# Kernel tuning notes

Measured on AMD Instinct MI355X. Metric: run time of the kernel, lower is better.

The kernel has to match this reference:

```python
import jax, jax.numpy as jnp
import numpy as np

N = 50000
E_RAND = 800000
IN_CH = 128
HID = 64
HEADS = 4
OUT_CH = 3
NEG_SLOPE = 0.2
BN_EPS = 1e-5


def setup_inputs() -> dict:
    key = jax.random.key(0)
    ks = jax.random.split(key, 24)
    x = jax.random.normal(ks[0], (N, IN_CH), dtype=jnp.float32)
    er = jax.random.randint(ks[1], (2, E_RAND), 0, N)
    sl = jnp.tile(jnp.arange(N, dtype=er.dtype)[None, :], (2, 1))
    edge_index = jnp.concatenate([er, sl], axis=1)  # [2, 850000]
    s = 0.1
    d1 = HID * HEADS            # 256
    d2 = (HID // 2) * HEADS     # 128
    inp = dict(x=x, edge_index=edge_index)
    # layer 1: in 128 -> heads*64
    inp["W1"] = s * jax.random.normal(ks[2], (IN_CH, HEADS * HID), dtype=jnp.float32)
    inp["a1s"] = s * jax.random.normal(ks[3], (HEADS, HID), dtype=jnp.float32)
    inp["a1d"] = s * jax.random.normal(ks[4], (HEADS, HID), dtype=jnp.float32)
    inp["b1"] = jnp.zeros((d1,), jnp.float32)
    inp["g1"] = jnp.ones((d1,), jnp.float32)
    inp["be1"] = jnp.zeros((d1,), jnp.float32)
    inp["m1"] = 0.01 * jax.random.normal(ks[5], (d1,), dtype=jnp.float32)
    inp["v1"] = jnp.ones((d1,), jnp.float32) + 0.01 * jax.random.uniform(ks[6], (d1,))
    # layer 2: in 256 -> heads*32
    inp["W2"] = s * jax.random.normal(ks[7], (d1, HEADS * (HID // 2)), dtype=jnp.float32)
    inp["a2s"] = s * jax.random.normal(ks[8], (HEADS, HID // 2), dtype=jnp.float32)
    inp["a2d"] = s * jax.random.normal(ks[9], (HEADS, HID // 2), dtype=jnp.float32)
    inp["b2"] = jnp.zeros((d2,), jnp.float32)
    inp["g2"] = jnp.ones((d2,), jnp.float32)
    inp["be2"] = jnp.zeros((d2,), jnp.float32)
    inp["m2"] = 0.01 * jax.random.normal(ks[10], (d2,), dtype=jnp.float32)
    inp["v2"] = jnp.ones((d2,), jnp.float32) + 0.01 * jax.random.uniform(ks[11], (d2,))
    # layer 3: in 128 -> 1 head, out_ch, concat=False
    inp["W3"] = s * jax.random.normal(ks[12], (d2, OUT_CH), dtype=jnp.float32)
    inp["a3s"] = s * jax.random.normal(ks[13], (1, OUT_CH), dtype=jnp.float32)
    inp["a3d"] = s * jax.random.normal(ks[14], (1, OUT_CH), dtype=jnp.float32)
    inp["b3"] = jnp.zeros((OUT_CH,), jnp.float32)
    return inp


def gat_conv(x, src, dst, W, a_src, a_dst, b, heads, fdim, concat):
    n = x.shape[0]
    h = (x @ W).reshape(n, heads, fdim)           # [N,H,F]
    als = jnp.einsum('nhf,hf->nh', h, a_src)      # [N,H]
    ald = jnp.einsum('nhf,hf->nh', h, a_dst)
    e = jax.nn.leaky_relu(als[src] + ald[dst], NEG_SLOPE)  # [E,H]
    m = jax.lax.stop_gradient(jax.ops.segment_max(e, dst, num_segments=n))
    ex = jnp.exp(e - m[dst])
    ssum = jax.ops.segment_sum(ex, dst, num_segments=n)
    alpha = ex / (ssum[dst] + 1e-16)              # segment softmax over in-edges
    msg = h[src] * alpha[:, :, None]              # [E,H,F]
    out = jax.ops.segment_sum(msg, dst, num_segments=n)  # [N,H,F]
    out = out.reshape(n, heads * fdim) if concat else out.mean(axis=1)
    return out + b


def batch_norm(x, gamma, beta, mean, var):
    return (x - mean) * jax.lax.rsqrt(var + BN_EPS) * gamma + beta


def reference(x, edge_index, W1, a1s, a1d, b1, g1, be1, m1, v1,
              W2, a2s, a2d, b2, g2, be2, m2, v2,
              W3, a3s, a3d, b3):
    src, dst = edge_index[0], edge_index[1]
    h = gat_conv(x, src, dst, W1, a1s, a1d, b1, HEADS, HID, True)
    h = jax.nn.elu(batch_norm(h, g1, be1, m1, v1))
    h = gat_conv(h, src, dst, W2, a2s, a2d, b2, HEADS, HID // 2, True)
    h = jax.nn.elu(batch_norm(h, g2, be2, m2, v2))
    h = gat_conv(h, src, dst, W3, a3s, a3d, b3, 1, OUT_CH, False)
    return jax.nn.log_softmax(h, axis=1)
```

## Files before the change

kernel.cpp:

```cpp
#include <hip/hip_runtime.h>


#define WSZ 64

typedef short short8 __attribute__((ext_vector_type(8)));
typedef short short4v __attribute__((ext_vector_type(4)));
typedef float float4v __attribute__((ext_vector_type(4)));

__device__ inline unsigned short f2bf(float f) {
  unsigned u = __float_as_uint(f);
  u += 0x7FFFu + ((u >> 16) & 1u);
  return (unsigned short)(u >> 16);
}
__device__ inline float bf2f(unsigned short u) {
  return __uint_as_float(((unsigned)u) << 16);
}


__global__ __launch_bounds__(256) void hist_kernel(const int* __restrict__ dst, int E,
                                                   int* __restrict__ deg) {
  int e = blockIdx.x * 256 + threadIdx.x;
  if (e < E) atomicAdd(&deg[dst[e]], 1);
}

__global__ __launch_bounds__(256) void block_sums_kernel(const int* __restrict__ deg, int n,
                                                         int* __restrict__ bsum) {
  __shared__ int sh[256];
  int t = threadIdx.x;
  int base = blockIdx.x * 1024 + t * 4;
  int v = 0;
#pragma unroll
  for (int j = 0; j < 4; ++j) {
    int idx = base + j;
    if (idx < n) v += deg[idx];
  }
  sh[t] = v;
  __syncthreads();
  for (int off = 128; off >= 1; off >>= 1) {
    if (t < off) sh[t] += sh[t + off];
    __syncthreads();
  }
  if (t == 0) bsum[blockIdx.x] = sh[0];
}

__global__ void tiny_scan_kernel(int* bsum, int nb) {
  if (threadIdx.x == 0 && blockIdx.x == 0) {
    int run = 0;
    for (int i = 0; i < nb; ++i) {
      int v = bsum[i];
      bsum[i] = run;
      run += v;
    }
  }
}

__global__ __launch_bounds__(256) void scan_write_kernel(const int* __restrict__ deg, int n,
                                                         const int* __restrict__ bbase,
                                                         int* __restrict__ row_start,
                                                         int* __restrict__ cursor) {
  __shared__ int sh[256];
  int t = threadIdx.x;
  int base = blockIdx.x * 1024 + t * 4;
  int v[4];
  int s = 0;
#pragma unroll
  for (int j = 0; j < 4; ++j) {
    int idx = base + j;
    v[j] = (idx < n) ? deg[idx] : 0;
    s += v[j];
  }
  sh[t] = s;
  __syncthreads();
  for (int off = 1; off < 256; off <<= 1) {
    int x = (t >= off) ? sh[t - off] : 0;
    __syncthreads();
    sh[t] += x;
    __syncthreads();
  }
  int excl = sh[t] - s + bbase[blockIdx.x];
#pragma unroll
  for (int j = 0; j < 4; ++j) {
    int idx = base + j;
    if (idx < n) {
      row_start[idx] = excl;
      cursor[idx] = excl;
    }
    excl += v[j];
  }
  if (blockIdx.x == gridDim.x - 1 && t == 255) row_start[n] = excl;
}

__global__ __launch_bounds__(256) void scatter_kernel(const int* __restrict__ src,
                                                      const int* __restrict__ dst, int E,
                                                      int* __restrict__ cursor,
                                                      int* __restrict__ csr_src) {
  int e = blockIdx.x * 256 + threadIdx.x;
  if (e < E) {
    int d = dst[e];
    int p = atomicAdd(&cursor[d], 1);
    csr_src[p] = src[e];
  }
}


__global__ __launch_bounds__(256) void conv_w1t_kernel(const float* __restrict__ W1,
                                                       unsigned short* __restrict__ W1t) {
  int idx = blockIdx.x * 256 + threadIdx.x;
  int n = idx >> 7, k = idx & 127;
  W1t[idx] = f2bf(W1[k * 256 + n]);
}

__global__ __launch_bounds__(256) void conv_w2t_kernel(const float* __restrict__ W2,
                                                       unsigned short* __restrict__ W2t) {
  int idx = blockIdx.x * 256 + threadIdx.x;
  int n = idx >> 8, p = idx & 255;
  int kl = (p & ~63) | ((p & 3) << 4) | ((p >> 2) & 15);
  W2t[idx] = f2bf(W2[kl * 128 + n]);
}


template <int K, int BN, bool AF32>
__global__ __launch_bounds__(256) void gemm_mfma(
    const void* __restrict__ Ap,
    const unsigned short* __restrict__ Bt,
    const float* __restrict__ a_s, const float* __restrict__ a_d,
    unsigned short* __restrict__ hout,
    float* __restrict__ als, float* __restrict__ ald,
    int M) {
  constexpr int CF = BN / 64;
  constexpr int PAD = 36;
  __shared__ unsigned short As[64][PAD];
  __shared__ unsigned short Bs[BN][PAD];
  const int t = threadIdx.x;
  const int w = t >> 6;
  const int lane = t & 63;
  const int c16 = lane & 15;
  const int q = lane >> 4;
  const int bm = blockIdx.x * 64;
  const int arow = t >> 2;
  const int akc = (t & 3) * 8;

  float4v acc[4][CF];
#pragma unroll
  for (int rf = 0; rf < 4; ++rf)
#pragma unroll
    for (int cf = 0; cf < CF; ++cf) acc[rf][cf] = float4v{0.f, 0.f, 0.f, 0.f};

  for (int k0 = 0; k0 < K; k0 += 32) {
    {
      int gr = bm + arow;
      if constexpr (AF32) {
        const float* Af = (const float*)Ap + (size_t)gr * K + k0 + akc;
        float4 v0 = make_float4(0.f, 0.f, 0.f, 0.f), v1 = v0;
        if (gr < M) {
          v0 = *(const float4*)Af;
          v1 = *(const float4*)(Af + 4);
        }
        ushort4 u0, u1;
        u0.x = f2bf(v0.x); u0.y = f2bf(v0.y); u0.z = f2bf(v0.z); u0.w = f2bf(v0.w);
        u1.x = f2bf(v1.x); u1.y = f2bf(v1.y); u1.z = f2bf(v1.z); u1.w = f2bf(v1.w);
        *(ushort4*)&As[arow][akc] = u0;
        *(ushort4*)&As[arow][akc + 4] = u1;
      } else {
        uint4 v = make_uint4(0u, 0u, 0u, 0u);
        if (gr < M) v = *(const uint4*)((const unsigned short*)Ap + (size_t)gr * K + k0 + akc);
        *(uint2*)&As[arow][akc] = make_uint2(v.x, v.y);
        *(uint2*)&As[arow][akc + 4] = make_uint2(v.z, v.w);
      }
    }
#pragma unroll
    for (int h = 0; h < BN / 64; ++h) {
      int n = (t >> 2) + h * 64;
      uint4 v = *(const uint4*)(Bt + (size_t)n * K + k0 + akc);
      *(uint2*)&Bs[n][akc] = make_uint2(v.x, v.y);
      *(uint2*)&Bs[n][akc + 4] = make_uint2(v.z, v.w);
    }
    __syncthreads();
    short8 af[4], bfr[CF];
#pragma unroll
    for (int rf = 0; rf < 4; ++rf) {
      short4v lo = *(short4v*)&As[rf * 16 + c16][q * 8];
      short4v hi = *(short4v*)&As[rf * 16 + c16][q * 8 + 4];
      af[rf] = __builtin_shufflevector(lo, hi, 0, 1, 2, 3, 4, 5, 6, 7);
    }
#pragma unroll
    for (int cf = 0; cf < CF; ++cf) {
      int n = w * (CF * 16) + cf * 16 + c16;
      short4v lo = *(short4v*)&Bs[n][q * 8];
      short4v hi = *(short4v*)&Bs[n][q * 8 + 4];
      bfr[cf] = __builtin_shufflevector(lo, hi, 0, 1, 2, 3, 4, 5, 6, 7);
    }
#pragma unroll
    for (int rf = 0; rf < 4; ++rf)
#pragma unroll
      for (int cf = 0; cf < CF; ++cf)
        acc[rf][cf] =
            __builtin_amdgcn_mfma_f32_16x16x32_bf16(af[rf], bfr[cf], acc[rf][cf], 0, 0, 0);
    __syncthreads();
  }

  float sasv[CF], sadv[CF];
#pragma unroll
  for (int cf = 0; cf < CF; ++cf) {
    int L = w * (CF * 16) + cf * 16 + c16;
    sasv[cf] = a_s[L];
    sadv[cf] = a_d[L];
  }
#pragma unroll
  for (int rf = 0; rf < 4; ++rf) {
#pragma unroll
    for (int r = 0; r < 4; ++r) {
      int n = bm + rf * 16 + q * 4 + r;
      float ps = 0.f, pd = 0.f;
      unsigned short us[CF];
#pragma unroll
      for (int cf = 0; cf < CF; ++cf) {
        float v = acc[rf][cf][r];
        us[cf] = f2bf(v);
        ps += v * sasv[cf];
        pd += v * sadv[cf];
      }
#pragma unroll
      for (int off = 1; off <= 8; off <<= 1) {
        ps += __shfl_xor(ps, off, 16);
        pd += __shfl_xor(pd, off, 16);
      }
      if (n < M) {
        if constexpr (CF == 4) {
          ushort4 u;
          u.x = us[0]; u.y = us[1]; u.z = us[2]; u.w = us[3];
          *(ushort4*)(hout + (size_t)n * BN + w * 64 + c16 * 4) = u;
        } else {
          ushort2 u;
          u.x = us[0]; u.y = us[1];
          *(ushort2*)(hout + (size_t)n * BN + w * 32 + c16 * 2) = u;
        }
        if (c16 == 0) {
          als[(size_t)n * 4 + w] = ps;
          ald[(size_t)n * 4 + w] = pd;
        }
      }
    }
  }
}


template <int D, bool FUSEL3>
__global__ __launch_bounds__(256) void gat_aggregate(
    const unsigned short* __restrict__ h_bf, const float* __restrict__ als,
    const float* __restrict__ ald, const int* __restrict__ row_start,
    const int* __restrict__ csr_src, const float* __restrict__ bias,
    const float* __restrict__ gamma, const float* __restrict__ beta,
    const float* __restrict__ bmean, const float* __restrict__ bvar,
    unsigned short* __restrict__ obf,
    const float* __restrict__ W3, const float* __restrict__ a3s,
    const float* __restrict__ a3d, float4* __restrict__ h3p,
    float* __restrict__ ald3,
    int n_nodes) {
  constexpr int VPT = D / WSZ;
  constexpr int H = 4;
  __shared__ float w3s[384];
  __shared__ float sa3[6];
  if constexpr (FUSEL3) {
    for (int i = threadIdx.x; i < 384; i += 256) w3s[i] = W3[i];
    if (threadIdx.x < 3) {
      sa3[threadIdx.x] = a3s[threadIdx.x];
      sa3[3 + threadIdx.x] = a3d[threadIdx.x];
    }
    __syncthreads();
  }
  int wid = threadIdx.x >> 6, lane = threadIdx.x & 63;
  int n = __builtin_amdgcn_readfirstlane(blockIdx.x * 4 + wid);
  if (n >= n_nodes) return;
  int hd = lane >> 4;
  const unsigned coff = (unsigned)(lane * VPT * 2);
  const unsigned aoff = (unsigned)(hd * 4);
  const char* hb = (const char*)h_bf;
  const char* ab = (const char*)als;
  float aldv = ald[(size_t)n * H + hd];
  int row = __builtin_amdgcn_readfirstlane(row_start[n]);
  int end = __builtin_amdgcn_readfirstlane(row_start[n + 1]);
  float acc[VPT] = {};
  float ssum = 0.f;
  int i = row;

#define EDGE_BLOCK(B)                                                          \
  for (; i + (B) <= end; i += (B)) {                                           \
    int s[B];                                                                  \
    _Pragma("unroll") for (int j = 0; j < (B); ++j) s[j] =                     \
        __builtin_amdgcn_readfirstlane(csr_src[i + j]);                        \
    float e[B];                                                                \
    _Pragma("unroll") for (int j = 0; j < (B); ++j) e[j] =                     \
        *(const float*)(ab + ((unsigned)s[j] * 16u + aoff)) + aldv;            \
    if constexpr (VPT == 4) {                                                  \
      ushort4 u[B];                                                            \
      _Pragma("unroll") for (int j = 0; j < (B); ++j) u[j] =                   \
          *(const ushort4*)(hb + ((unsigned)s[j] * (unsigned)(D * 2) + coff)); \
      _Pragma("unroll") for (int j = 0; j < (B); ++j) {                        \
        float ee = fmaxf(e[j], 0.2f * e[j]);                                   \
        float ex = __expf(ee);                                                 \
        ssum += ex;                                                            \
        acc[0] += ex * bf2f(u[j].x);                                           \
        acc[1] += ex * bf2f(u[j].y);                                           \
        acc[2] += ex * bf2f(u[j].z);                                           \
        acc[3] += ex * bf2f(u[j].w);                                           \
      }                                                                        \
    } else {                                                                   \
      ushort2 u[B];                                                            \
      _Pragma("unroll") for (int j = 0; j < (B); ++j) u[j] =                   \
          *(const ushort2*)(hb + ((unsigned)s[j] * (unsigned)(D * 2) + coff)); \
      _Pragma("unroll") for (int j = 0; j < (B); ++j) {                        \
        float ee = fmaxf(e[j], 0.2f * e[j]);                                   \
        float ex = __expf(ee);                                                 \
        ssum += ex;                                                            \
        acc[0] += ex * bf2f(u[j].x);                                           \
        acc[1] += ex * bf2f(u[j].y);                                           \
      }                                                                        \
    }                                                                          \
  }

  EDGE_BLOCK(8)
  EDGE_BLOCK(4)
  EDGE_BLOCK(1)
#undef EDGE_BLOCK

  float inv = 1.f / (ssum + 1e-16f);
#pragma unroll
  for (int j = 0; j < VPT; ++j) {
    int cl = hd * (VPT * 16) + j * 16 + (lane & 15);
    float o = acc[j] * inv + bias[cl];
    o = (o - bmean[cl]) * rsqrtf(bvar[cl] + 1e-5f) * gamma[cl] + beta[cl];
    o = (o > 0.f) ? o : (__expf(o) - 1.f);
    acc[j] = o;
  }
  if constexpr (!FUSEL3) {
    ushort4 u;
    u.x = f2bf(acc[0]); u.y = f2bf(acc[1]); u.z = f2bf(acc[2]); u.w = f2bf(acc[3]);
    *(ushort4*)(obf + (size_t)n * D + (lane * VPT)) = u;
  } else {
    int k0l = hd * 32 + (lane & 15);
    int k1l = k0l + 16;
    float p0 = acc[0] * w3s[k0l * 3 + 0] + acc[1] * w3s[k1l * 3 + 0];
    float p1 = acc[0] * w3s[k0l * 3 + 1] + acc[1] * w3s[k1l * 3 + 1];
    float p2 = acc[0] * w3s[k0l * 3 + 2] + acc[1] * w3s[k1l * 3 + 2];
#pragma unroll
    for (int off = 32; off >= 1; off >>= 1) {
      p0 += __shfl_xor(p0, off, 64);
      p1 += __shfl_xor(p1, off, 64);
      p2 += __shfl_xor(p2, off, 64);
    }
    if (lane == 0) {
      float als3 = p0 * sa3[0] + p1 * sa3[1] + p2 * sa3[2];
      float ad3 = p0 * sa3[3] + p1 * sa3[4] + p2 * sa3[5];
      h3p[n] = make_float4(p0, p1, p2, als3);
      ald3[n] = ad3;
    }
  }
}


__global__ __launch_bounds__(256) void l3_agg_kernel(const float4* __restrict__ h3p,
                                                     const float* __restrict__ ald3,
                                                     const int* __restrict__ row_start,
                                                     const int* __restrict__ csr_src,
                                                     const float* __restrict__ b3,
                                                     float* __restrict__ out, int n_nodes) {
  int wid = threadIdx.x >> 6, lane = threadIdx.x & 63;
  int n = __builtin_amdgcn_readfirstlane(blockIdx.x * 4 + wid);
  if (n >= n_nodes) return;
  float aldv = ald3[n];
  int row = __builtin_amdgcn_readfirstlane(row_start[n]);
  int end = __builtin_amdgcn_readfirstlane(row_start[n + 1]);
  const char* hp = (const char*)h3p;
  float a0 = 0.f, a1 = 0.f, a2 = 0.f, ss = 0.f;
  for (int i = row + lane; i < end; i += 64) {
    int s = csr_src[i];
    float4 hv = *(const float4*)(hp + ((unsigned)s * 16u));
    float e = hv.w + aldv;
    e = fmaxf(e, 0.2f * e);
    float ex = __expf(e);
    ss += ex;
    a0 += ex * hv.x;
    a1 += ex * hv.y;
    a2 += ex * hv.z;
  }
#pragma unroll
  for (int off = 32; off >= 1; off >>= 1) {
    a0 += __shfl_xor(a0, off, 64);
    a1 += __shfl_xor(a1, off, 64);
    a2 += __shfl_xor(a2, off, 64);
    ss += __shfl_xor(ss, off, 64);
  }
  if (lane == 0) {
    float inv = 1.f / (ss + 1e-16f);
    float o0 = a0 * inv + b3[0];
    float o1 = a1 * inv + b3[1];
    float o2 = a2 * inv + b3[2];
    float m = fmaxf(o0, fmaxf(o1, o2));
    float lse = m + logf(expf(o0 - m) + expf(o1 - m) + expf(o2 - m));
    out[n * 3 + 0] = o0 - lse;
    out[n * 3 + 1] = o1 - lse;
    out[n * 3 + 2] = o2 - lse;
  }
}


extern "C" void kernel_launch(void* const* d_in, const int* in_sizes, int n_in,
                              void* d_out, int out_size, void* d_ws, size_t ws_size,
                              hipStream_t stream) {
  const float* x   = (const float*)d_in[0];
  const int*   ei  = (const int*)d_in[1];
  const float* W1  = (const float*)d_in[2];
  const float* a1s = (const float*)d_in[3];
  const float* a1d = (const float*)d_in[4];
  const float* b1  = (const float*)d_in[5];
  const float* g1v = (const float*)d_in[6];
  const float* be1 = (const float*)d_in[7];
  const float* m1  = (const float*)d_in[8];
  const float* v1  = (const float*)d_in[9];
  const float* W2  = (const float*)d_in[10];
  const float* a2s = (const float*)d_in[11];
  const float* a2d = (const float*)d_in[12];
  const float* b2  = (const float*)d_in[13];
  const float* g2v = (const float*)d_in[14];
  const float* be2 = (const float*)d_in[15];
  const float* m2  = (const float*)d_in[16];
  const float* v2  = (const float*)d_in[17];
  const float* W3  = (const float*)d_in[18];
  const float* a3s = (const float*)d_in[19];
  const float* a3d = (const float*)d_in[20];
  const float* b3  = (const float*)d_in[21];
  float* out = (float*)d_out;

  const int N = in_sizes[0] / 128;
  const int E = in_sizes[1] / 2;
  const int* srcv = ei;
  const int* dstv = ei + E;

  float* wsf  = (float*)d_ws;
  float* als1 = wsf;
  float* ald1 = als1 + (size_t)N * 4;
  float* als2 = ald1 + (size_t)N * 4;
  float* ald2 = als2 + (size_t)N * 4;
  float* h3p  = ald2 + (size_t)N * 4;
  float* ald3 = h3p + (size_t)N * 4;
  unsigned short* h_bf1 = (unsigned short*)(ald3 + N);
  unsigned short* o1_bf = h_bf1 + (size_t)N * 256;
  unsigned short* h_bf2 = o1_bf + (size_t)N * 256;
  unsigned short* W1t   = h_bf2 + (size_t)N * 128;
  unsigned short* W2t   = W1t + 256 * 128;
  int* deg       = (int*)(W2t + 128 * 256);
  int* row_start = deg + N;
  int* cursor    = row_start + (N + 1);
  int* csr_src   = cursor + (N + 1);
  int* bsum      = csr_src + E;

  const int eb = (E + 255) / 256;
  const int nb = (N + 1023) / 1024;
  const int nodes4 = (N + 3) / 4;
  const int mblocks = (N + 63) / 64;

  conv_w1t_kernel<<<128, 256, 0, stream>>>(W1, W1t);
  conv_w2t_kernel<<<128, 256, 0, stream>>>(W2, W2t);

  hipMemsetAsync(deg, 0, (size_t)N * sizeof(int), stream);
  hist_kernel<<<eb, 256, 0, stream>>>(dstv, E, deg);
  block_sums_kernel<<<nb, 256, 0, stream>>>(deg, N, bsum);
  tiny_scan_kernel<<<1, 64, 0, stream>>>(bsum, nb);
  scan_write_kernel<<<nb, 256, 0, stream>>>(deg, N, bsum, row_start, cursor);
  scatter_kernel<<<eb, 256, 0, stream>>>(srcv, dstv, E, cursor, csr_src);

  gemm_mfma<128, 256, true><<<mblocks, 256, 0, stream>>>(x, W1t, a1s, a1d, h_bf1, als1,
                                                         ald1, N);
  gat_aggregate<256, false><<<nodes4, 256, 0, stream>>>(
      h_bf1, als1, ald1, row_start, csr_src, b1, g1v, be1, m1, v1, o1_bf, nullptr, nullptr,
      nullptr, nullptr, nullptr, N);
  gemm_mfma<256, 128, false><<<mblocks, 256, 0, stream>>>(o1_bf, W2t, a2s, a2d, h_bf2, als2,
                                                          ald2, N);
  gat_aggregate<128, true><<<nodes4, 256, 0, stream>>>(
      h_bf2, als2, ald2, row_start, csr_src, b2, g2v, be2, m2, v2, nullptr, W3, a3s, a3d,
      (float4*)h3p, ald3, N);
  l3_agg_kernel<<<nodes4, 256, 0, stream>>>((const float4*)h3p, ald3, row_start, csr_src,
                                            b3, out, N);
}
```

Measured before the change: 385.9 us.

## Store GAT features as feature slices and aggregate per slice block

The GEMM epilogue now writes hidden features into 8 feature-slice planes, each contiguous per node. The aggregation kernels assign each block one slice and a group of 8 nodes, processing several edges in parallel per wave with lane groups, so gathers touch a smaller working set that may fit in cache. Layer-3 prep is split into a separate kernel that reads an fp32 intermediate. The cost is redundant reads of CSR and attention logits across 8 slices, plus an extra kernel and an fp32 round trip.

```diff
diff --git a/kernel.cpp b/kernel.cpp
--- a/kernel.cpp
+++ b/kernel.cpp
@@ -6,6 +6,7 @@
 typedef short short8 __attribute__((ext_vector_type(8)));
 typedef short short4v __attribute__((ext_vector_type(4)));
 typedef float float4v __attribute__((ext_vector_type(4)));
+typedef float f2v __attribute__((ext_vector_type(2)));
 
 __device__ inline unsigned short f2bf(float f) {
   unsigned u = __float_as_uint(f);
@@ -128,6 +129,7 @@
     float* __restrict__ als, float* __restrict__ ald,
     int M) {
   constexpr int CF = BN / 64;
+  constexpr int SF = BN / 8;
   constexpr int PAD = 36;
   __shared__ unsigned short As[64][PAD];
   __shared__ unsigned short Bs[BN][PAD];
@@ -206,6 +208,7 @@
     sasv[cf] = a_s[L];
     sadv[cf] = a_d[L];
   }
+  const size_t sub = (size_t)(w * 2 + (c16 >> 3)) * (size_t)M * SF;
 #pragma unroll
   for (int rf = 0; rf < 4; ++rf) {
 #pragma unroll
@@ -229,11 +232,11 @@
         if constexpr (CF == 4) {
           ushort4 u;
           u.x = us[0]; u.y = us[1]; u.z = us[2]; u.w = us[3];
-          *(ushort4*)(hout + (size_t)n * BN + w * 64 + c16 * 4) = u;
+          *(ushort4*)(hout + sub + (size_t)n * 32 + (c16 & 7) * 4) = u;
         } else {
           ushort2 u;
           u.x = us[0]; u.y = us[1];
-          *(ushort2*)(hout + (size_t)n * BN + w * 32 + c16 * 2) = u;
+          *(ushort2*)(hout + sub + (size_t)n * 16 + (c16 & 7) * 2) = u;
         }
         if (c16 == 0) {
           als[(size_t)n * 4 + w] = ps;
@@ -245,116 +248,128 @@
 }
 
 
-template <int D, bool FUSEL3>
-__global__ __launch_bounds__(256) void gat_aggregate(
-    const unsigned short* __restrict__ h_bf, const float* __restrict__ als,
-    const float* __restrict__ ald, const int* __restrict__ row_start,
-    const int* __restrict__ csr_src, const float* __restrict__ bias,
-    const float* __restrict__ gamma, const float* __restrict__ beta,
-    const float* __restrict__ bmean, const float* __restrict__ bvar,
+template <int D>
+__global__ __launch_bounds__(256) void gat_agg_slice(
+    const unsigned short* __restrict__ h_sl,
+    const float* __restrict__ als, const float* __restrict__ ald,
+    const int* __restrict__ row_start, const int* __restrict__ csr_src,
+    const float* __restrict__ bias, const float* __restrict__ gamma,
+    const float* __restrict__ beta, const float* __restrict__ bmean,
+    const float* __restrict__ bvar,
     unsigned short* __restrict__ obf,
-    const float* __restrict__ W3, const float* __restrict__ a3s,
-    const float* __restrict__ a3d, float4* __restrict__ h3p,
-    float* __restrict__ ald3,
+    float* __restrict__ of32,
     int n_nodes) {
-  constexpr int VPT = D / WSZ;
-  constexpr int H = 4;
+  constexpr int SFEAT = (D == 256) ? 32 : 16;
+  constexpr int FP = SFEAT / 2;
+  constexpr int EPG = 64 / FP;
+  const int b = blockIdx.x;
+  const int sl = b & 7;
+  const int g = b >> 3;
+  const int wid = threadIdx.x >> 6;
+  const int lane = threadIdx.x & 63;
+  const int f = lane & (FP - 1);
+  const int eg = lane >> ((D == 256) ? 4 : 3);
+  const int head = sl >> 1;
+  const char* hsb = (const char*)(h_sl + (size_t)sl * (size_t)n_nodes * SFEAT);
+  const char* ab = (const char*)als;
+
+  for (int rep = 0; rep < 2; ++rep) {
+    int n = __builtin_amdgcn_readfirstlane(g * 8 + wid + rep * 4);
+    if (n >= n_nodes) continue;
+    float aldv = ald[(size_t)n * 4 + head];
+    int row = __builtin_amdgcn_readfirstlane(row_start[n]);
+    int end = __builtin_amdgcn_readfirstlane(row_start[n + 1]);
+    float acc0 = 0.f, acc1 = 0.f, ssum = 0.f;
+    for (int i = row; i < end; i += EPG) {
+      int idx = i + eg;
+      idx = (idx < end) ? idx : (end - 1);
+      int s = __builtin_nontemporal_load(&csr_src[idx]);
+      float al = *(const float*)(ab + ((unsigned)s * 16u + (unsigned)(head * 4)));
+      unsigned u = *(const unsigned*)(hsb + ((unsigned)s * (unsigned)(SFEAT * 2) +
+                                             (unsigned)(f * 4)));
+      float e = al + aldv;
+      e = fmaxf(e, 0.2f * e);
+      float ex = __expf(e);
+      ex = (i + eg < end) ? ex : 0.f;
+      ssum += ex;
+      acc0 += ex * __uint_as_float(u << 16);
+      acc1 += ex * __uint_as_float(u & 0xffff0000u);
+    }
+    if constexpr (EPG == 8) {
+      ssum += __shfl_xor(ssum, 8, 64);
+      acc0 += __shfl_xor(acc0, 8, 64);
+      acc1 += __shfl_xor(acc1, 8, 64);
+    }
+    ssum += __shfl_xor(ssum, 16, 64);
+    acc0 += __shfl_xor(acc0, 16, 64);
+    acc1 += __shfl_xor(acc1, 16, 64);
+    ssum += __shfl_xor(ssum, 32, 64);
+    acc0 += __shfl_xor(acc0, 32, 64);
+    acc1 += __shfl_xor(acc1, 32, 64);
+    float inv = 1.f / (ssum + 1e-16f);
+    int l0, l1;
+    if constexpr (D == 256) {
+      l0 = head * 64 + ((f & 1) * 2 + 0) * 16 + (sl & 1) * 8 + (f >> 1);
+      l1 = head * 64 + ((f & 1) * 2 + 1) * 16 + (sl & 1) * 8 + (f >> 1);
+    } else {
+      l0 = head * 32 + (sl & 1) * 8 + f;
+      l1 = l0 + 16;
+    }
+    float o0 = acc0 * inv + bias[l0];
+    o0 = (o0 - bmean[l0]) * rsqrtf(bvar[l0] + 1e-5f) * gamma[l0] + beta[l0];
+    o0 = (o0 > 0.f) ? o0 : (__expf(o0) - 1.f);
+    float o1v = acc1 * inv + bias[l1];
+    o1v = (o1v - bmean[l1]) * rsqrtf(bvar[l1] + 1e-5f) * gamma[l1] + beta[l1];
+    o1v = (o1v > 0.f) ? o1v : (__expf(o1v) - 1.f);
+    if (eg == 0) {
+      if constexpr (D == 256) {
+        unsigned pk = (unsigned)f2bf(o0) | ((unsigned)f2bf(o1v) << 16);
+        __builtin_nontemporal_store(
+            pk, (unsigned*)(obf + (size_t)n * 256 + sl * 32 + f * 2));
+      } else {
+        f2v v2;
+        v2.x = o0; v2.y = o1v;
+        __builtin_nontemporal_store(
+            v2, (f2v*)(of32 + (size_t)n * 128 + sl * 16 + f * 2));
+      }
+    }
+  }
+}
+
+
+__global__ __launch_bounds__(256) void l3_prep_kernel(
+    const float* __restrict__ o2, const float* __restrict__ W3,
+    const float* __restrict__ a3s, const float* __restrict__ a3d,
+    float4* __restrict__ h3p, float* __restrict__ ald3, int n_nodes) {
   __shared__ float w3s[384];
   __shared__ float sa3[6];
-  if constexpr (FUSEL3) {
-    for (int i = threadIdx.x; i < 384; i += 256) w3s[i] = W3[i];
-    if (threadIdx.x < 3) {
-      sa3[threadIdx.x] = a3s[threadIdx.x];
-      sa3[3 + threadIdx.x] = a3d[threadIdx.x];
-    }
-    __syncthreads();
-  }
+  for (int i = threadIdx.x; i < 384; i += 256) w3s[i] = W3[i];
+  if (threadIdx.x < 3) {
+    sa3[threadIdx.x] = a3s[threadIdx.x];
+    sa3[3 + threadIdx.x] = a3d[threadIdx.x];
+  }
+  __syncthreads();
   int wid = threadIdx.x >> 6, lane = threadIdx.x & 63;
-  int n = __builtin_amdgcn_readfirstlane(blockIdx.x * 4 + wid);
+  int n = blockIdx.x * 4 + wid;
   if (n >= n_nodes) return;
+  f2v v = *(const f2v*)(o2 + (size_t)n * 128 + lane * 2);
   int hd = lane >> 4;
-  const unsigned coff = (unsigned)(lane * VPT * 2);
-  const unsigned aoff = (unsigned)(hd * 4);
-  const char* hb = (const char*)h_bf;
-  const char* ab = (const char*)als;
-  float aldv = ald[(size_t)n * H + hd];
-  int row = __builtin_amdgcn_readfirstlane(row_start[n]);
-  int end = __builtin_amdgcn_readfirstlane(row_start[n + 1]);
-  float acc[VPT] = {};
-  float ssum = 0.f;
-  int i = row;
-
-#define EDGE_BLOCK(B)                                                          \
-  for (; i + (B) <= end; i += (B)) {                                           \
-    int s[B];                                                                  \
-    _Pragma("unroll") for (int j = 0; j < (B); ++j) s[j] =                     \
-        __builtin_amdgcn_readfirstlane(csr_src[i + j]);                        \
-    float e[B];                                                                \
-    _Pragma("unroll") for (int j = 0; j < (B); ++j) e[j] =                     \
-        *(const float*)(ab + ((unsigned)s[j] * 16u + aoff)) + aldv;            \
-    if constexpr (VPT == 4) {                                                  \
-      ushort4 u[B];                                                            \
-      _Pragma("unroll") for (int j = 0; j < (B); ++j) u[j] =                   \
-          *(const ushort4*)(hb + ((unsigned)s[j] * (unsigned)(D * 2) + coff)); \
-      _Pragma("unroll") for (int j = 0; j < (B); ++j) {                        \
-        float ee = fmaxf(e[j], 0.2f * e[j]);                                   \
-        float ex = __expf(ee);                                                 \
-        ssum += ex;                                                            \
-        acc[0] += ex * bf2f(u[j].x);                                           \
-        acc[1] += ex * bf2f(u[j].y);                                           \
-        acc[2] += ex * bf2f(u[j].z);                                           \
-        acc[3] += ex * bf2f(u[j].w);                                           \
-      }                                                                        \
-    } else {                                                                   \
-      ushort2 u[B];                                                            \
-      _Pragma("unroll") for (int j = 0; j < (B); ++j) u[j] =                   \
-          *(const ushort2*)(hb + ((unsigned)s[j] * (unsigned)(D * 2) + coff)); \
-      _Pragma("unroll") for (int j = 0; j < (B); ++j) {                        \
-        float ee = fmaxf(e[j], 0.2f * e[j]);                                   \
-        float ex = __expf(ee);                                                 \
-        ssum += ex;                                                            \
-        acc[0] += ex * bf2f(u[j].x);                                           \
-        acc[1] += ex * bf2f(u[j].y);                                           \
-      }                                                                        \
-    }                                                                          \
-  }
-
-  EDGE_BLOCK(8)
-  EDGE_BLOCK(4)
-  EDGE_BLOCK(1)
-#undef EDGE_BLOCK
-
-  float inv = 1.f / (ssum + 1e-16f);
-#pragma unroll
-  for (int j = 0; j < VPT; ++j) {
-    int cl = hd * (VPT * 16) + j * 16 + (lane & 15);
-    float o = acc[j] * inv + bias[cl];
-    o = (o - bmean[cl]) * rsqrtf(bvar[cl] + 1e-5f) * gamma[cl] + beta[cl];
-    o = (o > 0.f) ? o : (__expf(o) - 1.f);
-    acc[j] = o;
-  }
-  if constexpr (!FUSEL3) {
-    ushort4 u;
-    u.x = f2bf(acc[0]); u.y = f2bf(acc[1]); u.z = f2bf(acc[2]); u.w = f2bf(acc[3]);
-    *(ushort4*)(obf + (size_t)n * D + (lane * VPT)) = u;
-  } else {
-    int k0l = hd * 32 + (lane & 15);
-    int k1l = k0l + 16;
-    float p0 = acc[0] * w3s[k0l * 3 + 0] + acc[1] * w3s[k1l * 3 + 0];
-    float p1 = acc[0] * w3s[k0l * 3 + 1] + acc[1] * w3s[k1l * 3 + 1];
-    float p2 = acc[0] * w3s[k0l * 3 + 2] + acc[1] * w3s[k1l * 3 + 2];
-#pragma unroll
-    for (int off = 32; off >= 1; off >>= 1) {
-      p0 += __shfl_xor(p0, off, 64);
-      p1 += __shfl_xor(p1, off, 64);
-      p2 += __shfl_xor(p2, off, 64);
-    }
-    if (lane == 0) {
-      float als3 = p0 * sa3[0] + p1 * sa3[1] + p2 * sa3[2];
-      float ad3 = p0 * sa3[3] + p1 * sa3[4] + p2 * sa3[5];
-      h3p[n] = make_float4(p0, p1, p2, als3);
-      ald3[n] = ad3;
-    }
+  int k0l = hd * 32 + (lane & 15);
+  int k1l = k0l + 16;
+  float p0 = v.x * w3s[k0l * 3 + 0] + v.y * w3s[k1l * 3 + 0];
+  float p1 = v.x * w3s[k0l * 3 + 1] + v.y * w3s[k1l * 3 + 1];
+  float p2 = v.x * w3s[k0l * 3 + 2] + v.y * w3s[k1l * 3 + 2];
+#pragma unroll
+  for (int off = 32; off >= 1; off >>= 1) {
+    p0 += __shfl_xor(p0, off, 64);
+    p1 += __shfl_xor(p1, off, 64);
+    p2 += __shfl_xor(p2, off, 64);
+  }
+  if (lane == 0) {
+    float als3 = p0 * sa3[0] + p1 * sa3[1] + p2 * sa3[2];
+    float ad3 = p0 * sa3[3] + p1 * sa3[4] + p2 * sa3[5];
+    h3p[n] = make_float4(p0, p1, p2, als3);
+    ald3[n] = ad3;
   }
 }
 
@@ -444,21 +459,23 @@
   float* ald2 = als2 + (size_t)N * 4;
   float* h3p  = ald2 + (size_t)N * 4;
   float* ald3 = h3p + (size_t)N * 4;
-  unsigned short* h_bf1 = (unsigned short*)(ald3 + N);
-  unsigned short* o1_bf = h_bf1 + (size_t)N * 256;
-  unsigned short* h_bf2 = o1_bf + (size_t)N * 256;
-  unsigned short* W1t   = h_bf2 + (size_t)N * 128;
+  unsigned short* h1s   = (unsigned short*)(ald3 + N);
+  unsigned short* o1_bf = h1s + (size_t)N * 256;
+  unsigned short* h2s   = o1_bf + (size_t)N * 256;
+  unsigned short* W1t   = h2s + (size_t)N * 128;
   unsigned short* W2t   = W1t + 256 * 128;
   int* deg       = (int*)(W2t + 128 * 256);
   int* row_start = deg + N;
   int* cursor    = row_start + (N + 1);
   int* csr_src   = cursor + (N + 1);
   int* bsum      = csr_src + E;
+  float* o2f = (float*)h1s;
 
   const int eb = (E + 255) / 256;
   const int nb = (N + 1023) / 1024;
   const int nodes4 = (N + 3) / 4;
   const int mblocks = (N + 63) / 64;
+  const int sliceblocks = ((N + 7) / 8) * 8;
 
   conv_w1t_kernel<<<128, 256, 0, stream>>>(W1, W1t);
   conv_w2t_kernel<<<128, 256, 0, stream>>>(W2, W2t);
@@ -470,16 +487,15 @@
   scan_write_kernel<<<nb, 256, 0, stream>>>(deg, N, bsum, row_start, cursor);
   scatter_kernel<<<eb, 256, 0, stream>>>(srcv, dstv, E, cursor, csr_src);
 
-  gemm_mfma<128, 256, true><<<mblocks, 256, 0, stream>>>(x, W1t, a1s, a1d, h_bf1, als1,
+  gemm_mfma<128, 256, true><<<mblocks, 256, 0, stream>>>(x, W1t, a1s, a1d, h1s, als1,
                                                          ald1, N);
-  gat_aggregate<256, false><<<nodes4, 256, 0, stream>>>(
-      h_bf1, als1, ald1, row_start, csr_src, b1, g1v, be1, m1, v1, o1_bf, nullptr, nullptr,
-      nullptr, nullptr, nullptr, N);
-  gemm_mfma<256, 128, false><<<mblocks, 256, 0, stream>>>(o1_bf, W2t, a2s, a2d, h_bf2, als2,
+  gat_agg_slice<256><<<sliceblocks, 256, 0, stream>>>(
+      h1s, als1, ald1, row_start, csr_src, b1, g1v, be1, m1, v1, o1_bf, nullptr, N);
+  gemm_mfma<256, 128, false><<<mblocks, 256, 0, stream>>>(o1_bf, W2t, a2s, a2d, h2s, als2,
                                                           ald2, N);
-  gat_aggregate<128, true><<<nodes4, 256, 0, stream>>>(
-      h_bf2, als2, ald2, row_start, csr_src, b2, g2v, be2, m2, v2, nullptr, W3, a3s, a3d,
-      (float4*)h3p, ald3, N);
+  gat_agg_slice<128><<<sliceblocks, 256, 0, stream>>>(
+      h2s, als2, ald2, row_start, csr_src, b2, g2v, be2, m2, v2, nullptr, o2f, N);
+  l3_prep_kernel<<<nodes4, 256, 0, stream>>>(o2f, W3, a3s, a3d, (float4*)h3p, ald3, N);
   l3_agg_kernel<<<nodes4, 256, 0, stream>>>((const float4*)h3p, ald3, row_start, csr_src,
                                             b3, out, N);
 }
```

Result: slower. 657.1 us (+70.3%).
